# Performance work log

Measured on AMD Instinct MI355X. Metric: run time of the kernel, lower is better.

## Reference

```python
import jax, jax.numpy as jnp
import numpy as np
import math

HEAD_DIM = 64
N_NEWTON_ITER = 6


def _top_k_sum_selection(T, select_number, mask):
    # T: [B,H,N,D]; mask: [B,N] int (True/1 => masked out for selection, per source)
    B, H, N, D = T.shape
    big = jnp.finfo(T.dtype).max
    # select_type == 'sum' -> non-absolute row sums over feature dim, excluding token 0
    somme = jnp.sum(T[:, :, 1:, :], axis=-1)                      # [B,H,N-1]
    somme = jnp.where(mask[:, None, 1:].astype(bool), -big, somme)
    top = jax.lax.top_k(somme, select_number - 1)[1] + 1          # [B,H,M-1]
    top = jnp.concatenate(
        [top, jnp.zeros((B, H, 1), dtype=top.dtype)], axis=-1)    # always keep token 0
    index = jnp.sort(top, axis=-1)                                 # [B,H,M]
    nt = jnp.take_along_axis(T, index[..., None], axis=2)          # [B,H,M,D]
    return nt, index


def _m_matrix_composition(C, r_index):
    # C: [B,H,N,M]; r_index: [B,H,M] -> gather selected rows -> [B,H,M,M]
    return jnp.take_along_axis(C, r_index[..., None], axis=2)


def _iterative_inv(mat, n_iter=N_NEWTON_ITER):
    M = mat.shape[-1]
    I = jnp.eye(M, dtype=mat.dtype)
    Km = mat
    # init_option == 'original': global max of column sums
    V = (1.0 / jnp.max(jnp.sum(Km, axis=-2))) * jnp.swapaxes(Km, -1, -2)
    for _ in range(n_iter):
        KV = jnp.matmul(Km, V)
        V = jnp.matmul(0.25 * V,
                       13.0 * I - jnp.matmul(KV, 15.0 * I - jnp.matmul(KV, 7.0 * I - KV)))
    return V


def setup_inputs() -> dict:
    key = jax.random.key(0)
    k1, k2, k3, k4 = jax.random.split(key, 4)
    B, H, N, D = 4, 8, 4096, 64
    return {
        "Q": jax.random.normal(k1, (B, H, N, D), dtype=jnp.float32),
        "K": jax.random.normal(k2, (B, H, N, D), dtype=jnp.float32),
        "V": jax.random.normal(k3, (B, H, N, D), dtype=jnp.float32),
        "mask": jax.random.randint(k4, (B, N), 0, 2, dtype=jnp.int32),
        "select_number": 64,
    }


def reference(Q, K, V, mask, select_number):
    big = jnp.finfo(Q.dtype).max
    Qs = Q / math.sqrt(HEAD_DIM)
    nc, _ = _top_k_sum_selection(K, select_number, mask)           # [B,H,M,D]
    nr, r_index = _top_k_sum_selection(Qs, select_number, mask)    # [B,H,M,D]
    c = jnp.einsum('bhnd,bhmd->bhnm', Qs, nc)                      # [B,H,N,M]
    r = jnp.einsum('bhmd,bhnd->bhmn', nr, K)                       # [B,H,M,N]
    # forward path fills where ~mask (mask==0 => masked)
    r = jnp.where(mask[:, None, None, :].astype(bool), r, -big)
    kernel_1 = jax.nn.softmax(c, axis=-1)                          # [B,H,N,M]
    u = _m_matrix_composition(kernel_1, r_index)                   # [B,H,M,M]
    kernel_3 = jax.nn.softmax(r, axis=-1)                          # [B,H,M,N]
    kernel_2_inv = _iterative_inv(u)                               # [B,H,M,M]
    X = jnp.matmul(kernel_1, jnp.matmul(kernel_2_inv, jnp.matmul(kernel_3, V)))
    return X
```

## Files before the change

kernel.cpp:

```cpp
#include <hip/hip_runtime.h>
#include <float.h>

#define BB 4
#define HH 8
#define BHN 32
#define NTOK 4096
#define DD 64
#define MM 64
#define PAD 68
#define GPART 16

typedef _Float16 f16;
typedef __attribute__((ext_vector_type(4))) _Float16 f16x4;
typedef __attribute__((ext_vector_type(8))) _Float16 f16x8;
typedef __attribute__((ext_vector_type(4))) float f32x4;

union V8U { f16x8 v; f16x4 q[2]; };

__device__ __forceinline__ void fsplit(float v, f16* h, f16* l) {
  f16 hh = (f16)v;
  *h = hh;
  *l = (f16)(v - (float)hh);
}

__device__ __forceinline__ f32x4 mm2(f16x8 a0, f16x8 a1, f16x8 b0, f16x8 b1) {
  f32x4 c = {0.f, 0.f, 0.f, 0.f};
  c = __builtin_amdgcn_mfma_f32_16x16x32_f16(a0, b0, c, 0, 0, 0);
  c = __builtin_amdgcn_mfma_f32_16x16x32_f16(a1, b1, c, 0, 0, 0);
  return c;
}

template<int LDA, int LDB>
__device__ __forceinline__ void mm_acc(float acc[4][4],
    const float (*A)[LDA], const float (*B)[LDB], int ti, int tj) {
  #pragma unroll
  for (int k4 = 0; k4 < 16; ++k4) {
    float a[4][4], b[4][4];
    #pragma unroll
    for (int x = 0; x < 4; ++x) {
      float4 t = *(const float4*)&A[ti*4+x][k4*4];
      a[x][0]=t.x; a[x][1]=t.y; a[x][2]=t.z; a[x][3]=t.w;
    }
    #pragma unroll
    for (int kk = 0; kk < 4; ++kk) {
      float4 t = *(const float4*)&B[k4*4+kk][tj*4];
      b[kk][0]=t.x; b[kk][1]=t.y; b[kk][2]=t.z; b[kk][3]=t.w;
    }
    #pragma unroll
    for (int kk = 0; kk < 4; ++kk)
      #pragma unroll
      for (int x = 0; x < 4; ++x)
        #pragma unroll
        for (int y = 0; y < 4; ++y)
          acc[x][y] = fmaf(a[x][kk], b[kk][y], acc[x][y]);
  }
}

__global__ __launch_bounds__(256) void k_somme(const float* __restrict__ Kg,
    const float* __restrict__ Qg, const int* __restrict__ mask,
    float* __restrict__ somK, float* __restrict__ somQ) {
  int tid = threadIdx.x;
  int lane = tid & 63;
  long grow = (long)blockIdx.x * 16 + (tid >> 6) * 4 + (lane >> 4);
  int which = grow >= (long)(BHN * NTOK);
  long row = which ? grow - (long)BHN * NTOK : grow;
  int n = (int)(row & (NTOK - 1));
  int bh = (int)(row >> 12);
  int b = bh >> 3;
  const float* src = which ? Qg : Kg;
  float4 v = *((const float4*)(src + row * DD) + (lane & 15));
  float s = v.x + v.y + v.z + v.w;
  s += __shfl_xor(s, 1); s += __shfl_xor(s, 2);
  s += __shfl_xor(s, 4); s += __shfl_xor(s, 8);
  if ((lane & 15) == 0) {
    float out = (n == 0 || mask[b * NTOK + n] != 0) ? -FLT_MAX : s;
    (which ? somQ : somK)[row] = out;
  }
}

__global__ __launch_bounds__(256) void k_select(const float* __restrict__ Kg,
    const float* __restrict__ Qg, const float* __restrict__ somK,
    const float* __restrict__ somQ, float* __restrict__ nc, float* __restrict__ nr,
    unsigned int* __restrict__ sync0) {
  int bh = blockIdx.x;
  int which = blockIdx.y;
  if (which == 0 && bh == 0 && threadIdx.x == 0) {
    #pragma unroll
    for (int i = 0; i < 34; ++i) sync0[i] = 0u;
  }
  __shared__ unsigned int keys[NTOK];
  __shared__ unsigned int wb[4][256];
  __shared__ int wsum[4];
  __shared__ int wsumB[4];
  __shared__ int sh_bin, sh_need;
  __shared__ int sel[MM];
  int tid = threadIdx.x, wave = tid >> 6, lane = tid & 63;
  const float* som = (which ? somQ : somK) + (long)bh * NTOK;
  for (int i = tid; i < NTOK; i += 256) {
    float f = som[i];
    unsigned int u = __float_as_uint(f);
    u = (u & 0x80000000u) ? ~u : (u | 0x80000000u);
    keys[i] = (i == 0) ? 0u : u;
  }
  unsigned int pref = 0; int need = MM - 1;
  for (int pass = 0; pass < 4; ++pass) {
    int shift = 24 - pass * 8;
    unsigned int pm = (pass == 0) ? 0u : (0xFFFFFFFFu << (32 - 8 * pass));
    unsigned int* wbf = (unsigned int*)wb;
    wbf[tid] = 0; wbf[tid + 256] = 0; wbf[tid + 512] = 0; wbf[tid + 768] = 0;
    __syncthreads();
    for (int i = tid; i < NTOK; i += 256) {
      unsigned int k = keys[i];
      if ((k & pm) == pref) atomicAdd(&wb[wave][(k >> shift) & 255], 1u);
    }
    __syncthreads();
    int binr = 255 - tid;
    int cnt = (int)(wb[0][binr] + wb[1][binr] + wb[2][binr] + wb[3][binr]);
    int v = cnt;
    #pragma unroll
    for (int d = 1; d < 64; d <<= 1) {
      int t = __shfl_up(v, d);
      if (lane >= d) v += t;
    }
    if (lane == 63) wsum[wave] = v;
    __syncthreads();
    int off = 0;
    #pragma unroll
    for (int w = 0; w < 4; ++w) off += (w < wave) ? wsum[w] : 0;
    v += off;
    int above = v - cnt;
    if (v >= need && above < need) { sh_bin = binr; sh_need = need - above; }
    __syncthreads();
    pref |= ((unsigned int)sh_bin) << shift;
    need = sh_need;
  }
  unsigned int thr = pref;

  int base = tid * 16;
  int ctie = 0;
  #pragma unroll
  for (int j = 0; j < 16; ++j) ctie += (keys[base + j] == thr);
  int v2 = ctie;
  #pragma unroll
  for (int d = 1; d < 64; d <<= 1) {
    int t = __shfl_up(v2, d);
    if (lane >= d) v2 += t;
  }
  if (lane == 63) wsum[wave] = v2;
  __syncthreads();
  int offt = 0;
  #pragma unroll
  for (int w = 0; w < 4; ++w) offt += (w < wave) ? wsum[w] : 0;
  int tie_excl = v2 + offt - ctie;

  int tieoff = tie_excl, cnt2 = 0;
  #pragma unroll
  for (int j = 0; j < 16; ++j) {
    unsigned int k = keys[base + j];
    int f = (k > thr) ? 1 : 0;
    if (k == thr) { f = (tieoff < need) ? 1 : 0; ++tieoff; }
    if (base + j == 0) f = 1;
    cnt2 += f;
  }
  int v3 = cnt2;
  #pragma unroll
  for (int d = 1; d < 64; d <<= 1) {
    int t = __shfl_up(v3, d);
    if (lane >= d) v3 += t;
  }
  if (lane == 63) wsumB[wave] = v3;
  __syncthreads();
  int offc = 0;
  #pragma unroll
  for (int w = 0; w < 4; ++w) offc += (w < wave) ? wsumB[w] : 0;
  int o = v3 + offc - cnt2;
  tieoff = tie_excl;
  #pragma unroll
  for (int j = 0; j < 16; ++j) {
    unsigned int k = keys[base + j];
    int f = (k > thr) ? 1 : 0;
    if (k == thr) { f = (tieoff < need) ? 1 : 0; ++tieoff; }
    if (base + j == 0) f = 1;
    if (f) sel[o++] = base + j;
  }
  __syncthreads();

  const float* src = which ? Qg : Kg;
  float* dst = (which ? nr : nc) + (long)bh * MM * DD;
  float scale = which ? 0.125f : 1.0f;
  for (int e = tid; e < MM * 16; e += 256) {
    int i = e >> 4, d4 = e & 15;
    float4 v = *(const float4*)&src[((long)bh * NTOK + sel[i]) * DD + d4 * 4];
    v.x *= scale; v.y *= scale; v.z *= scale; v.w *= scale;
    *(float4*)&dst[i * DD + d4 * 4] = v;
  }
}

__device__ void newton_fused(char* smem, const float* __restrict__ nc,
    const float* __restrict__ nr, unsigned int* __restrict__ scal,
    unsigned int* __restrict__ uflag, const float* __restrict__ nump,
    const float* __restrict__ denp, unsigned int* __restrict__ w3cnt,
    float* __restrict__ Zg, int bh) {
  int tid = threadIdx.x;
  float* uL = (float*)(smem + 55296);

  {
    float (*A)[PAD] = (float(*)[PAD])smem;
    float (*BT)[MM] = (float(*)[MM])(smem + 17408);
    float (*cs)[MM] = (float(*)[MM])(smem + 33792);
    if (tid < 256) {
      for (int e = tid; e < 1024; e += 256) {
        int m = e >> 4, d4 = e & 15;
        *(float4*)&A[m][d4*4] = *(const float4*)&nr[(long)bh*MM*DD + m*DD + d4*4];
        float4 c = *(const float4*)&nc[(long)bh*MM*DD + m*DD + d4*4];
        BT[d4*4+0][m] = c.x; BT[d4*4+1][m] = c.y; BT[d4*4+2][m] = c.z; BT[d4*4+3][m] = c.w;
      }
    }
    __syncthreads();
    if (tid < 256) {
      int ti = tid >> 4, tj = tid & 15;
      float acc[4][4] = {};
      mm_acc<PAD, MM>(acc, A, BT, ti, tj);
      float e_[4][4];
      #pragma unroll
      for (int x = 0; x < 4; ++x)
        #pragma unroll
        for (int y = 0; y < 4; ++y) e_[x][y] = expf(acc[x][y]);
      float rsx[4];
      #pragma unroll
      for (int x = 0; x < 4; ++x) {
        rsx[x] = e_[x][0] + e_[x][1] + e_[x][2] + e_[x][3];
        rsx[x] += __shfl_xor(rsx[x], 1); rsx[x] += __shfl_xor(rsx[x], 2);
        rsx[x] += __shfl_xor(rsx[x], 4); rsx[x] += __shfl_xor(rsx[x], 8);
      }
      float cp[4] = {0.f, 0.f, 0.f, 0.f};
      #pragma unroll
      for (int x = 0; x < 4; ++x) {
        float inv = 1.f / rsx[x];
        float v0 = e_[x][0]*inv, v1 = e_[x][1]*inv, v2 = e_[x][2]*inv, v3 = e_[x][3]*inv;
        cp[0] += v0; cp[1] += v1; cp[2] += v2; cp[3] += v3;
        float4 o; o.x = v0; o.y = v1; o.z = v2; o.w = v3;
        *(float4*)&uL[(ti*4+x)*MM + tj*4] = o;
      }
      #pragma unroll
      for (int y = 0; y < 4; ++y) {
        cp[y] += __shfl_xor(cp[y], 16);
        cp[y] += __shfl_xor(cp[y], 32);
      }
      if (((tid >> 4) & 3) == 0) {
        #pragma unroll
        for (int y = 0; y < 4; ++y) cs[tid >> 6][tj*4 + y] = cp[y];
      }
    }
    __syncthreads();
    if (tid < 64) {
      float tot = cs[0][tid] + cs[1][tid] + cs[2][tid] + cs[3][tid];
      for (int off = 32; off; off >>= 1) tot = fmaxf(tot, __shfl_xor(tot, off));
      if (tid == 0) atomicMax(scal, __float_as_uint(tot));
    }
    __syncthreads();
    if (tid == 0)
      __hip_atomic_fetch_add(uflag, 1u, __ATOMIC_RELEASE, __HIP_MEMORY_SCOPE_AGENT);
    if (tid == 0) {
      while (__hip_atomic_load(uflag, __ATOMIC_ACQUIRE, __HIP_MEMORY_SCOPE_AGENT) < 32u)
        __builtin_amdgcn_s_sleep(1);
      unsigned int sv = __hip_atomic_load(scal, __ATOMIC_RELAXED, __HIP_MEMORY_SCOPE_AGENT);
      cs[0][0] = 1.0f / __uint_as_float(sv);
    }
    __syncthreads();
  }
  float c0 = ((float(*)[MM])(smem + 33792))[0][0];
  __syncthreads();

  f16 (*VT_h)[72] = (f16(*)[72])(smem);
  f16 (*Vr_h)[72] = (f16(*)[72])(smem + 9216);
  f16 (*PT_h)[72] = (f16(*)[72])(smem + 18432);
  f16 (*PT_l)[72] = (f16(*)[72])(smem + 27648);
  f16 (*RT_h)[72] = (f16(*)[72])(smem + 36864);
  f16 (*RT_l)[72] = (f16(*)[72])(smem + 46080);
  float (*Vi)[PAD] = (float(*)[PAD])(smem + 36864);
  int wave = tid >> 6, lane = tid & 63;
  int wr = wave >> 1, wc = wave & 1;
  int lm = lane & 15, hi = lane >> 4;

  for (int e = tid; e < 4096; e += 512) {
    int i = e >> 6, j = e & 63;
    f16 h = (f16)(uL[e] * c0);
    VT_h[i][j] = h;
    Vr_h[j][i] = h;
  }
  f16x8 kb_h[2], kb_l[2];
  {
    const float* p = uL + (wr*16 + lm) * 64;
    float kv[16];
    *(float4*)&kv[0]  = *(const float4*)(p + hi*8);
    *(float4*)&kv[4]  = *(const float4*)(p + hi*8 + 4);
    *(float4*)&kv[8]  = *(const float4*)(p + 32 + hi*8);
    *(float4*)&kv[12] = *(const float4*)(p + 36 + hi*8);
    #pragma unroll
    for (int j = 0; j < 8; ++j) {
      f16 h, l;
      fsplit(kv[j], &h, &l);     kb_h[0][j] = h; kb_l[0][j] = l;
      fsplit(kv[8+j], &h, &l);   kb_h[1][j] = h; kb_l[1][j] = l;
    }
  }
  __syncthreads();

  for (int it = 0; it < 6; ++it) {
    const bool last = (it == 5);

    f32x4 st[4];
    #pragma unroll
    for (int g = 0; g < 4; ++g) {
      f16x8 a0 = *(const f16x8*)&VT_h[g*16 + lm][hi*8];
      f16x8 a1 = *(const f16x8*)&VT_h[g*16 + lm][32 + hi*8];
      f32x4 c = mm2(a0, a1, kb_h[0], kb_h[1]);
      if (last) {
        c = __builtin_amdgcn_mfma_f32_16x16x32_f16(a0, kb_l[0], c, 0, 0, 0);
        c = __builtin_amdgcn_mfma_f32_16x16x32_f16(a1, kb_l[1], c, 0, 0, 0);
      }
      st[g] = c;
    }
    f16x8 sa[2];
    #pragma unroll
    for (int g = 0; g < 4; ++g)
      #pragma unroll
      for (int r = 0; r < 4; ++r)
        sa[g >> 1][(g & 1)*4 + r] = (f16)st[g][r];
    #pragma unroll
    for (int g = 0; g < 4; ++g) {
      if ((g >> 1) == wc) {
        #pragma unroll
        for (int r = 0; r < 4; ++r) {
          int i = g*16 + hi*4 + r, j = wr*16 + lm;
          float pv = (i == j ? 7.f : 0.f) - st[g][r];
          if (last) {
            f16 h, l; fsplit(pv, &h, &l);
            PT_h[i][j] = h; PT_l[i][j] = l;
          } else {
            PT_h[i][j] = (f16)pv;
          }
        }
      }
    }
    __syncthreads();

    #pragma unroll
    for (int cc2 = 0; cc2 < 2; ++cc2) {
      int cc = wc*2 + cc2;
      V8U bh0, bh1;
      bh0.q[0] = *(const f16x4*)&PT_h[cc*16 + lm][hi*4];
      bh0.q[1] = *(const f16x4*)&PT_h[cc*16 + lm][16 + hi*4];
      bh1.q[0] = *(const f16x4*)&PT_h[cc*16 + lm][32 + hi*4];
      bh1.q[1] = *(const f16x4*)&PT_h[cc*16 + lm][48 + hi*4];
      f32x4 a = mm2(sa[0], sa[1], bh0.v, bh1.v);
      if (last) {
        V8U bl0, bl1;
        bl0.q[0] = *(const f16x4*)&PT_l[cc*16 + lm][hi*4];
        bl0.q[1] = *(const f16x4*)&PT_l[cc*16 + lm][16 + hi*4];
        bl1.q[0] = *(const f16x4*)&PT_l[cc*16 + lm][32 + hi*4];
        bl1.q[1] = *(const f16x4*)&PT_l[cc*16 + lm][48 + hi*4];
        a = __builtin_amdgcn_mfma_f32_16x16x32_f16(sa[0], bl0.v, a, 0, 0, 0);
        a = __builtin_amdgcn_mfma_f32_16x16x32_f16(sa[1], bl1.v, a, 0, 0, 0);
      }
      f16x4 wh, wl;
      #pragma unroll
      for (int r = 0; r < 4; ++r) {
        int row = wr*16 + hi*4 + r, col = cc*16 + lm;
        float rv = (row == col ? 15.f : 0.f) - a[r];
        if (last) { f16 h, l; fsplit(rv, &h, &l); wh[r] = h; wl[r] = l; }
        else wh[r] = (f16)rv;
      }
      *(f16x4*)&RT_h[cc*16 + lm][wr*16 + hi*4] = wh;
      if (last) *(f16x4*)&RT_l[cc*16 + lm][wr*16 + hi*4] = wl;
    }
    __syncthreads();

    #pragma unroll
    for (int cc2 = 0; cc2 < 2; ++cc2) {
      int cc = wc*2 + cc2;
      V8U bh0, bh1;
      bh0.q[0] = *(const f16x4*)&RT_h[cc*16 + lm][hi*4];
      bh0.q[1] = *(const f16x4*)&RT_h[cc*16 + lm][16 + hi*4];
      bh1.q[0] = *(const f16x4*)&RT_h[cc*16 + lm][32 + hi*4];
      bh1.q[1] = *(const f16x4*)&RT_h[cc*16 + lm][48 + hi*4];
      f32x4 a = mm2(sa[0], sa[1], bh0.v, bh1.v);
      if (last) {
        V8U bl0, bl1;
        bl0.q[0] = *(const f16x4*)&RT_l[cc*16 + lm][hi*4];
        bl0.q[1] = *(const f16x4*)&RT_l[cc*16 + lm][16 + hi*4];
        bl1.q[0] = *(const f16x4*)&RT_l[cc*16 + lm][32 + hi*4];
        bl1.q[1] = *(const f16x4*)&RT_l[cc*16 + lm][48 + hi*4];
        a = __builtin_amdgcn_mfma_f32_16x16x32_f16(sa[0], bl0.v, a, 0, 0, 0);
        a = __builtin_amdgcn_mfma_f32_16x16x32_f16(sa[1], bl1.v, a, 0, 0, 0);
      }
      f16x4 wh, wl;
      #pragma unroll
      for (int r = 0; r < 4; ++r) {
        int row = wr*16 + hi*4 + r, col = cc*16 + lm;
        float wv = (row == col ? 13.f : 0.f) - a[r];
        if (last) { f16 h, l; fsplit(wv, &h, &l); wh[r] = h; wl[r] = l; }
        else wh[r] = (f16)wv;
      }
      *(f16x4*)&PT_h[cc*16 + lm][wr*16 + hi*4] = wh;
      if (last) *(f16x4*)&PT_l[cc*16 + lm][wr*16 + hi*4] = wl;
    }
    __syncthreads();

    f16x8 vh0 = *(const f16x8*)&Vr_h[wr*16 + lm][hi*8];
    f16x8 vh1 = *(const f16x8*)&Vr_h[wr*16 + lm][32 + hi*8];
    #pragma unroll
    for (int cc2 = 0; cc2 < 2; ++cc2) {
      int cc = wc*2 + cc2;
      f16x8 wh0 = *(const f16x8*)&PT_h[cc*16 + lm][hi*8];
      f16x8 wh1 = *(const f16x8*)&PT_h[cc*16 + lm][32 + hi*8];
      f32x4 a = mm2(vh0, vh1, wh0, wh1);
      if (last) {
        f16x8 wl0 = *(const f16x8*)&PT_l[cc*16 + lm][hi*8];
        f16x8 wl1 = *(const f16x8*)&PT_l[cc*16 + lm][32 + hi*8];
        a = __builtin_amdgcn_mfma_f32_16x16x32_f16(vh0, wl0, a, 0, 0, 0);
        a = __builtin_amdgcn_mfma_f32_16x16x32_f16(vh1, wl1, a, 0, 0, 0);
        #pragma unroll
        for (int r = 0; r < 4; ++r)
          Vi[wr*16 + hi*4 + r][cc*16 + lm] = 0.25f * a[r];
      } else {
        f16x4 th;
        #pragma unroll
        for (int r = 0; r < 4; ++r) {
          f16 h = (f16)(0.25f * a[r]);
          Vr_h[wr*16 + hi*4 + r][cc*16 + lm] = h;
          th[r] = h;
        }
        *(f16x4*)&VT_h[cc*16 + lm][wr*16 + hi*4] = th;
      }
    }
    __syncthreads();
  }

  if (tid == 0) {
    while (__hip_atomic_load(&w3cnt[bh], __ATOMIC_ACQUIRE, __HIP_MEMORY_SCOPE_AGENT) < 8u)
      __builtin_amdgcn_s_sleep(1);
  }
  __syncthreads();
  float (*W)[PAD] = (float(*)[PAD])smem;
  float* dn = (float*)(smem + 54272);
  if (tid < 64) {
    float s = 0.f;
    #pragma unroll
    for (int g = 0; g < GPART; ++g) s += denp[((long)bh * GPART + g) * MM + tid];
    dn[tid] = s;
  }
  __syncthreads();
  for (int e = tid; e < 1024; e += 512) {
    int m = e >> 4, d4 = e & 15;
    float4 s = {0.f, 0.f, 0.f, 0.f};
    #pragma unroll
    for (int g = 0; g < GPART; ++g) {
      float4 t = *(const float4*)&nump[((long)bh * GPART + g) * (MM*DD) + m*DD + d4*4];
      s.x += t.x; s.y += t.y; s.z += t.z; s.w += t.w;
    }
    float inv = 1.f / dn[m];
    s.x *= inv; s.y *= inv; s.z *= inv; s.w *= inv;
    *(float4*)&W[m][d4*4] = s;
  }
  __syncthreads();
  if (tid < 256) {
    int ti = tid >> 4, tj = tid & 15;
    float acc[4][4] = {};
    mm_acc<PAD, PAD>(acc, Vi, W, ti, tj);
    #pragma unroll
    for (int x = 0; x < 4; ++x) {
      float4 o; o.x = acc[x][0]; o.y = acc[x][1]; o.z = acc[x][2]; o.w = acc[x][3];
      *(float4*)&Zg[(long)bh*MM*DD + (ti*4+x)*DD + tj*4] = o;
    }
  }
}

__device__ void w3_dev(char* smem, const float* __restrict__ Kg,
    const float* __restrict__ Vg, const int* __restrict__ maskg,
    const float* __restrict__ nr, float* __restrict__ nump,
    float* __restrict__ denp, unsigned int* __restrict__ w3cnt, int idx) {
  int bh = idx >> 3, grp = idx & 7, b = bh >> 3;
  int tid = threadIdx.x;
  int half = tid >> 8, t = tid & 255;
  f16 (*Ks)[72] = (f16(*)[72])(smem + half * 18432);
  f16 (*Vs)[72] = (f16(*)[72])(smem + half * 18432 + 9216);
  float* kmul = (float*)(smem + 36864) + half * 64;
  int lane = tid & 63;
  int lm = lane & 15, hi = lane >> 4;
  int wv = t >> 6;
  int m0 = wv * 16;
  int gslot = grp * 2 + half;

  f16x8 nrf[2];
  {
    const float* p = nr + (long)bh*MM*DD + (long)(m0 + lm)*DD + hi*8;
    float4 q0 = *(const float4*)p;
    float4 q1 = *(const float4*)(p + 4);
    float4 q2 = *(const float4*)(p + 32);
    float4 q3 = *(const float4*)(p + 36);
    nrf[0][0]=(f16)q0.x; nrf[0][1]=(f16)q0.y; nrf[0][2]=(f16)q0.z; nrf[0][3]=(f16)q0.w;
    nrf[0][4]=(f16)q1.x; nrf[0][5]=(f16)q1.y; nrf[0][6]=(f16)q1.z; nrf[0][7]=(f16)q1.w;
    nrf[1][0]=(f16)q2.x; nrf[1][1]=(f16)q2.y; nrf[1][2]=(f16)q2.z; nrf[1][3]=(f16)q2.w;
    nrf[1][4]=(f16)q3.x; nrf[1][5]=(f16)q3.y; nrf[1][6]=(f16)q3.z; nrf[1][7]=(f16)q3.w;
  }

  f32x4 nacc[4];
  #pragma unroll
  for (int dt = 0; dt < 4; ++dt) nacc[dt] = (f32x4){0.f, 0.f, 0.f, 0.f};
  float dsum = 0.f;

  for (int sc = 0; sc < 4; ++sc) {
    int n0c = (gslot * 4 + sc) * 64;
    if (sc) __syncthreads();
    for (int s = t; s < 1024; s += 256) {
      int row = s >> 4, c4 = s & 15;
      float4 kv = *(const float4*)&Kg[((long)bh*NTOK + n0c + row)*DD + c4*4];
      float4 vv = *(const float4*)&Vg[((long)bh*NTOK + n0c + row)*DD + c4*4];
      f16x4 kk = {(f16)kv.x, (f16)kv.y, (f16)kv.z, (f16)kv.w};
      f16x4 vv4 = {(f16)vv.x, (f16)vv.y, (f16)vv.z, (f16)vv.w};
      *(f16x4*)&Ks[row][c4*4] = kk;
      *(f16x4*)&Vs[row][c4*4] = vv4;
    }
    if (t < 64) kmul[t] = maskg[b * NTOK + n0c + t] ? 1.f : 0.f;
    __syncthreads();

    f32x4 stv[4];
    #pragma unroll
    for (int g = 0; g < 4; ++g) {
      f16x8 a0 = *(const f16x8*)&Ks[g*16 + lm][hi*8];
      f16x8 a1 = *(const f16x8*)&Ks[g*16 + lm][32 + hi*8];
      stv[g] = mm2(a0, a1, nrf[0], nrf[1]);
    }
    f16x8 pa[2];
    #pragma unroll
    for (int g = 0; g < 4; ++g) {
      #pragma unroll
      for (int r = 0; r < 4; ++r) {
        float p = __expf(stv[g][r]) * kmul[g*16 + hi*4 + r];
        dsum += p;
        pa[g >> 1][(g & 1)*4 + r] = (f16)p;
      }
    }
    #pragma unroll
    for (int dt = 0; dt < 4; ++dt) {
      f16x8 vb0, vb1;
      #pragma unroll
      for (int j = 0; j < 8; ++j) {
        int nrow = hi*4 + (j & 3) + 16*(j >> 2);
        vb0[j] = Vs[nrow][dt*16 + lm];
        vb1[j] = Vs[32 + nrow][dt*16 + lm];
      }
      nacc[dt] = __builtin_amdgcn_mfma_f32_16x16x32_f16(pa[0], vb0, nacc[dt], 0, 0, 0);
      nacc[dt] = __builtin_amdgcn_mfma_f32_16x16x32_f16(pa[1], vb1, nacc[dt], 0, 0, 0);
    }
  }
  float* pnum = nump + ((long)bh * GPART + gslot) * (MM * DD);
  #pragma unroll
  for (int dt = 0; dt < 4; ++dt)
    #pragma unroll
    for (int r = 0; r < 4; ++r)
      pnum[(m0 + hi*4 + r)*DD + dt*16 + lm] = nacc[dt][r];
  float d2 = dsum + __shfl_xor(dsum, 16);
  d2 += __shfl_xor(d2, 32);
  if (lane < 16)
    denp[((long)bh * GPART + gslot) * MM + m0 + lane] = d2;
  __syncthreads();
  if (tid == 0)
    __hip_atomic_fetch_add(&w3cnt[bh], 1u, __ATOMIC_RELEASE, __HIP_MEMORY_SCOPE_AGENT);
}

__global__ __launch_bounds__(512, 4) void k_fuse(
    const float* __restrict__ nc, const float* __restrict__ nr,
    unsigned int* __restrict__ scal, unsigned int* __restrict__ uflag,
    const float* __restrict__ Kg, const float* __restrict__ Vg,
    const int* __restrict__ maskg,
    float* __restrict__ nump, float* __restrict__ denp,
    unsigned int* __restrict__ w3cnt, float* __restrict__ Zg) {
  __shared__ __align__(16) char smem[71680];
  if (blockIdx.x < 32)
    newton_fused(smem, nc, nr, scal, uflag, nump, denp, w3cnt, Zg, blockIdx.x);
  else
    w3_dev(smem, Kg, Vg, maskg, nr, nump, denp, w3cnt, blockIdx.x - 32);
}

__global__ __launch_bounds__(256) void k_final(const float* __restrict__ Qg,
    const float* __restrict__ nc, const float* __restrict__ Zg, float* __restrict__ Xg) {
  int bh = blockIdx.x, chunk = blockIdx.y;
  int tid = threadIdx.x;
  int wave = tid >> 6, lane = tid & 63;
  int lm = lane & 15, hi = lane >> 4;
  int n0 = chunk * 64;
  __shared__ f16 Qs[64][72];
  __shared__ f16 Ncs[64][72];
  __shared__ f16 Zs[64][72];
  for (int s = tid; s < 1024; s += 256) {
    int row = s >> 4, c4 = s & 15;
    float4 q = *(const float4*)&Qg[((long)bh*NTOK + n0 + row)*DD + c4*4];
    f16x4 qq = {(f16)(q.x*0.125f), (f16)(q.y*0.125f), (f16)(q.z*0.125f), (f16)(q.w*0.125f)};
    *(f16x4*)&Qs[row][c4*4] = qq;
    float4 cv = *(const float4*)&nc[(long)bh*MM*DD + row*DD + c4*4];
    f16x4 cc = {(f16)cv.x, (f16)cv.y, (f16)cv.z, (f16)cv.w};
    *(f16x4*)&Ncs[row][c4*4] = cc;
    float4 zv = *(const float4*)&Zg[(long)bh*MM*DD + row*DD + c4*4];
    f16x4 zz = {(f16)zv.x, (f16)zv.y, (f16)zv.z, (f16)zv.w};
    *(f16x4*)&Zs[row][c4*4] = zz;
  }
  __syncthreads();

  f16x8 qb0 = *(const f16x8*)&Qs[wave*16 + lm][hi*8];
  f16x8 qb1 = *(const f16x8*)&Qs[wave*16 + lm][32 + hi*8];
  f32x4 stv[4];
  #pragma unroll
  for (int mt = 0; mt < 4; ++mt) {
    f16x8 a0 = *(const f16x8*)&Ncs[mt*16 + lm][hi*8];
    f16x8 a1 = *(const f16x8*)&Ncs[mt*16 + lm][32 + hi*8];
    stv[mt] = mm2(a0, a1, qb0, qb1);
  }
  f16x8 pa[2];
  float dsum = 0.f;
  #pragma unroll
  for (int mt = 0; mt < 4; ++mt) {
    #pragma unroll
    for (int r = 0; r < 4; ++r) {
      float p = __expf(stv[mt][r]);
      dsum += p;
      pa[mt >> 1][(mt & 1)*4 + r] = (f16)p;
    }
  }
  float dtot = dsum + __shfl_xor(dsum, 16);
  dtot += __shfl_xor(dtot, 32);
  f32x4 xacc[4];
  #pragma unroll
  for (int dt = 0; dt < 4; ++dt) {
    f16x8 zb0, zb1;
    #pragma unroll
    for (int j = 0; j < 8; ++j) {
      int mrow = hi*4 + (j & 3) + 16*(j >> 2);
      zb0[j] = Zs[mrow][dt*16 + lm];
      zb1[j] = Zs[32 + mrow][dt*16 + lm];
    }
    f32x4 c = {0.f, 0.f, 0.f, 0.f};
    c = __builtin_amdgcn_mfma_f32_16x16x32_f16(pa[0], zb0, c, 0, 0, 0);
    c = __builtin_amdgcn_mfma_f32_16x16x32_f16(pa[1], zb1, c, 0, 0, 0);
    xacc[dt] = c;
  }
  float rn[4];
  #pragma unroll
  for (int r = 0; r < 4; ++r) rn[r] = 1.f / __shfl(dtot, hi*4 + r);
  #pragma unroll
  for (int dt = 0; dt < 4; ++dt)
    #pragma unroll
    for (int r = 0; r < 4; ++r)
      Xg[((long)bh*NTOK + n0 + wave*16 + hi*4 + r)*DD + dt*16 + lm] = xacc[dt][r] * rn[r];
}

extern "C" void kernel_launch(void* const* d_in, const int* in_sizes, int n_in,
                              void* d_out, int out_size, void* d_ws, size_t ws_size,
                              hipStream_t stream) {
  (void)in_sizes; (void)n_in; (void)out_size; (void)ws_size;
  const float* Qp = (const float*)d_in[0];
  const float* Kp = (const float*)d_in[1];
  const float* Vp = (const float*)d_in[2];
  const int* maskp = (const int*)d_in[3];
  float* out = (float*)d_out;

  float* wsf = (float*)d_ws;
  float* NUMP = wsf;
  float* DENP = NUMP + (long)BHN * GPART * MM * DD;
  unsigned int* SYNC = (unsigned int*)(DENP + BHN * GPART * MM);
  float* NC = (float*)(SYNC + 64);
  float* NR = NC + BHN * MM * DD;
  float* Zb = NR + BHN * MM * DD;
  float* SK = Zb + BHN * MM * DD;
  float* SQ = SK + BHN * NTOK;

  unsigned int* SCAL = SYNC;
  unsigned int* UFLAG = SYNC + 1;
  unsigned int* W3CNT = SYNC + 2;

  k_somme<<<16384, 256, 0, stream>>>(Kp, Qp, maskp, SK, SQ);
  k_select<<<dim3(32, 2), 256, 0, stream>>>(Kp, Qp, SK, SQ, NC, NR, SYNC);
  k_fuse<<<32 + 256, 512, 0, stream>>>(NC, NR, SCAL, UFLAG, Kp, Vp, maskp,
                                       NUMP, DENP, W3CNT, Zb);
  k_final<<<dim3(32, 64), 256, 0, stream>>>(Qp, NC, Zb, out);
}
```

Before: 80.14 us.

## Move U-matrix softmax into select kernel, drop in-kernel grid barrier

k_select now uses one 512-thread block per head that selects both K and Q top-k together. It then builds the 64x64 softmax matrix u and the global column-sum max directly from shared memory and writes u to global memory. The Newton blocks in k_fuse read u and the scale instead of recomputing them, which removes the spin-wait barrier across 32 blocks and lowers the shared memory needed per block. Zeroing the sync counters moves into k_somme. In exchange, k_select becomes a heavier serial stage made of only 32 blocks.

```diff
diff --git a/kernel.cpp b/kernel.cpp
--- a/kernel.cpp
+++ b/kernel.cpp
@@ -58,8 +58,13 @@
 
 __global__ __launch_bounds__(256) void k_somme(const float* __restrict__ Kg,
     const float* __restrict__ Qg, const int* __restrict__ mask,
-    float* __restrict__ somK, float* __restrict__ somQ) {
+    float* __restrict__ somK, float* __restrict__ somQ,
+    unsigned int* __restrict__ syncp) {
   int tid = threadIdx.x;
+  if (blockIdx.x == 0 && tid == 0) {
+    #pragma unroll
+    for (int i = 0; i < 34; ++i) syncp[i] = 0u;
+  }
   int lane = tid & 63;
   long grow = (long)blockIdx.x * 16 + (tid >> 6) * 4 + (lane >> 4);
   int which = grow >= (long)(BHN * NTOK);
@@ -78,25 +83,22 @@
   }
 }
 
-__global__ __launch_bounds__(256) void k_select(const float* __restrict__ Kg,
+__global__ __launch_bounds__(512) void k_select(const float* __restrict__ Kg,
     const float* __restrict__ Qg, const float* __restrict__ somK,
     const float* __restrict__ somQ, float* __restrict__ nc, float* __restrict__ nr,
-    unsigned int* __restrict__ sync0) {
+    float* __restrict__ ug, unsigned int* __restrict__ scal) {
+  __shared__ __align__(16) char sm[40960];
+  __shared__ int wsum[2][4], wsumB[2][4], sh_bin[2], sh_need[2];
+  __shared__ int sel[2][MM];
   int bh = blockIdx.x;
-  int which = blockIdx.y;
-  if (which == 0 && bh == 0 && threadIdx.x == 0) {
-    #pragma unroll
-    for (int i = 0; i < 34; ++i) sync0[i] = 0u;
-  }
-  __shared__ unsigned int keys[NTOK];
-  __shared__ unsigned int wb[4][256];
-  __shared__ int wsum[4];
-  __shared__ int wsumB[4];
-  __shared__ int sh_bin, sh_need;
-  __shared__ int sel[MM];
-  int tid = threadIdx.x, wave = tid >> 6, lane = tid & 63;
-  const float* som = (which ? somQ : somK) + (long)bh * NTOK;
-  for (int i = tid; i < NTOK; i += 256) {
+  int tid = threadIdx.x;
+  int half = tid >> 8, t = tid & 255;
+  int lane = tid & 63, wv = (tid >> 6) & 3;
+  unsigned int* keys = (unsigned int*)sm + half * 4096;
+  unsigned int* wbp  = (unsigned int*)(sm + 32768) + half * 1024;
+
+  const float* som = (half ? somQ : somK) + (long)bh * NTOK;
+  for (int i = t; i < NTOK; i += 256) {
     float f = som[i];
     unsigned int u = __float_as_uint(f);
     u = (u & 0x80000000u) ? ~u : (u | 0x80000000u);
@@ -106,51 +108,50 @@
   for (int pass = 0; pass < 4; ++pass) {
     int shift = 24 - pass * 8;
     unsigned int pm = (pass == 0) ? 0u : (0xFFFFFFFFu << (32 - 8 * pass));
-    unsigned int* wbf = (unsigned int*)wb;
-    wbf[tid] = 0; wbf[tid + 256] = 0; wbf[tid + 512] = 0; wbf[tid + 768] = 0;
-    __syncthreads();
-    for (int i = tid; i < NTOK; i += 256) {
+    wbp[t] = 0; wbp[t + 256] = 0; wbp[t + 512] = 0; wbp[t + 768] = 0;
+    __syncthreads();
+    for (int i = t; i < NTOK; i += 256) {
       unsigned int k = keys[i];
-      if ((k & pm) == pref) atomicAdd(&wb[wave][(k >> shift) & 255], 1u);
-    }
-    __syncthreads();
-    int binr = 255 - tid;
-    int cnt = (int)(wb[0][binr] + wb[1][binr] + wb[2][binr] + wb[3][binr]);
+      if ((k & pm) == pref) atomicAdd(&wbp[wv * 256 + ((k >> shift) & 255)], 1u);
+    }
+    __syncthreads();
+    int binr = 255 - t;
+    int cnt = (int)(wbp[binr] + wbp[256 + binr] + wbp[512 + binr] + wbp[768 + binr]);
     int v = cnt;
     #pragma unroll
     for (int d = 1; d < 64; d <<= 1) {
-      int t = __shfl_up(v, d);
-      if (lane >= d) v += t;
-    }
-    if (lane == 63) wsum[wave] = v;
+      int tt = __shfl_up(v, d);
+      if (lane >= d) v += tt;
+    }
+    if (lane == 63) wsum[half][wv] = v;
     __syncthreads();
     int off = 0;
     #pragma unroll
-    for (int w = 0; w < 4; ++w) off += (w < wave) ? wsum[w] : 0;
+    for (int w = 0; w < 4; ++w) off += (w < wv) ? wsum[half][w] : 0;
     v += off;
     int above = v - cnt;
-    if (v >= need && above < need) { sh_bin = binr; sh_need = need - above; }
-    __syncthreads();
-    pref |= ((unsigned int)sh_bin) << shift;
-    need = sh_need;
+    if (v >= need && above < need) { sh_bin[half] = binr; sh_need[half] = need - above; }
+    __syncthreads();
+    pref |= ((unsigned int)sh_bin[half]) << shift;
+    need = sh_need[half];
   }
   unsigned int thr = pref;
 
-  int base = tid * 16;
+  int base = t * 16;
   int ctie = 0;
   #pragma unroll
   for (int j = 0; j < 16; ++j) ctie += (keys[base + j] == thr);
   int v2 = ctie;
   #pragma unroll
   for (int d = 1; d < 64; d <<= 1) {
-    int t = __shfl_up(v2, d);
-    if (lane >= d) v2 += t;
-  }
-  if (lane == 63) wsum[wave] = v2;
+    int tt = __shfl_up(v2, d);
+    if (lane >= d) v2 += tt;
+  }
+  if (lane == 63) wsum[half][wv] = v2;
   __syncthreads();
   int offt = 0;
   #pragma unroll
-  for (int w = 0; w < 4; ++w) offt += (w < wave) ? wsum[w] : 0;
+  for (int w = 0; w < 4; ++w) offt += (w < wv) ? wsum[half][w] : 0;
   int tie_excl = v2 + offt - ctie;
 
   int tieoff = tie_excl, cnt2 = 0;
@@ -165,14 +166,14 @@
   int v3 = cnt2;
   #pragma unroll
   for (int d = 1; d < 64; d <<= 1) {
-    int t = __shfl_up(v3, d);
-    if (lane >= d) v3 += t;
-  }
-  if (lane == 63) wsumB[wave] = v3;
+    int tt = __shfl_up(v3, d);
+    if (lane >= d) v3 += tt;
+  }
+  if (lane == 63) wsumB[half][wv] = v3;
   __syncthreads();
   int offc = 0;
   #pragma unroll
-  for (int w = 0; w < 4; ++w) offc += (w < wave) ? wsumB[w] : 0;
+  for (int w = 0; w < 4; ++w) offc += (w < wv) ? wsumB[half][w] : 0;
   int o = v3 + offc - cnt2;
   tieoff = tie_excl;
   #pragma unroll
@@ -181,97 +182,77 @@
     int f = (k > thr) ? 1 : 0;
     if (k == thr) { f = (tieoff < need) ? 1 : 0; ++tieoff; }
     if (base + j == 0) f = 1;
-    if (f) sel[o++] = base + j;
-  }
-  __syncthreads();
-
-  const float* src = which ? Qg : Kg;
-  float* dst = (which ? nr : nc) + (long)bh * MM * DD;
-  float scale = which ? 0.125f : 1.0f;
-  for (int e = tid; e < MM * 16; e += 256) {
+    if (f) sel[half][o++] = base + j;
+  }
+  __syncthreads();
+
+  float (*A)[PAD] = (float(*)[PAD])sm;
+  float (*BT)[MM] = (float(*)[MM])(sm + 17408);
+  float (*cs)[MM] = (float(*)[MM])(sm + 33792);
+  const float* src = half ? Qg : Kg;
+  float* dst = (half ? nr : nc) + (long)bh * MM * DD;
+  float scale = half ? 0.125f : 1.0f;
+  for (int e = t; e < 1024; e += 256) {
     int i = e >> 4, d4 = e & 15;
-    float4 v = *(const float4*)&src[((long)bh * NTOK + sel[i]) * DD + d4 * 4];
+    float4 v = *(const float4*)&src[((long)bh * NTOK + sel[half][i]) * DD + d4 * 4];
     v.x *= scale; v.y *= scale; v.z *= scale; v.w *= scale;
     *(float4*)&dst[i * DD + d4 * 4] = v;
-  }
-}
-
-__device__ void newton_fused(char* smem, const float* __restrict__ nc,
-    const float* __restrict__ nr, unsigned int* __restrict__ scal,
-    unsigned int* __restrict__ uflag, const float* __restrict__ nump,
+    if (half) {
+      *(float4*)&A[i][d4*4] = v;
+    } else {
+      BT[d4*4+0][i] = v.x; BT[d4*4+1][i] = v.y;
+      BT[d4*4+2][i] = v.z; BT[d4*4+3][i] = v.w;
+    }
+  }
+  __syncthreads();
+
+  if (tid < 256) {
+    int ti = tid >> 4, tj = tid & 15;
+    float acc[4][4] = {};
+    mm_acc<PAD, MM>(acc, A, BT, ti, tj);
+    float e_[4][4];
+    #pragma unroll
+    for (int x = 0; x < 4; ++x)
+      #pragma unroll
+      for (int y = 0; y < 4; ++y) e_[x][y] = expf(acc[x][y]);
+    float rsx[4];
+    #pragma unroll
+    for (int x = 0; x < 4; ++x) {
+      rsx[x] = e_[x][0] + e_[x][1] + e_[x][2] + e_[x][3];
+      rsx[x] += __shfl_xor(rsx[x], 1); rsx[x] += __shfl_xor(rsx[x], 2);
+      rsx[x] += __shfl_xor(rsx[x], 4); rsx[x] += __shfl_xor(rsx[x], 8);
+    }
+    float cp[4] = {0.f, 0.f, 0.f, 0.f};
+    #pragma unroll
+    for (int x = 0; x < 4; ++x) {
+      float inv = 1.f / rsx[x];
+      float v0 = e_[x][0]*inv, v1 = e_[x][1]*inv, v2 = e_[x][2]*inv, v3 = e_[x][3]*inv;
+      cp[0] += v0; cp[1] += v1; cp[2] += v2; cp[3] += v3;
+      float4 ov; ov.x = v0; ov.y = v1; ov.z = v2; ov.w = v3;
+      *(float4*)&ug[(long)bh*MM*MM + (ti*4+x)*MM + tj*4] = ov;
+    }
+    #pragma unroll
+    for (int y = 0; y < 4; ++y) {
+      cp[y] += __shfl_xor(cp[y], 16);
+      cp[y] += __shfl_xor(cp[y], 32);
+    }
+    if (((tid >> 4) & 3) == 0) {
+      #pragma unroll
+      for (int y = 0; y < 4; ++y) cs[tid >> 6][tj*4 + y] = cp[y];
+    }
+  }
+  __syncthreads();
+  if (tid < 64) {
+    float tot = cs[0][tid] + cs[1][tid] + cs[2][tid] + cs[3][tid];
+    for (int off = 32; off; off >>= 1) tot = fmaxf(tot, __shfl_xor(tot, off));
+    if (tid == 0) atomicMax(scal, __float_as_uint(tot));
+  }
+}
+
+__device__ void newton_fused(char* smem, const float* __restrict__ ug,
+    const unsigned int* __restrict__ scal, const float* __restrict__ nump,
     const float* __restrict__ denp, unsigned int* __restrict__ w3cnt,
     float* __restrict__ Zg, int bh) {
-  int tid = threadIdx.x;
-  float* uL = (float*)(smem + 55296);
-
-  {
-    float (*A)[PAD] = (float(*)[PAD])smem;
-    float (*BT)[MM] = (float(*)[MM])(smem + 17408);
-    float (*cs)[MM] = (float(*)[MM])(smem + 33792);
-    if (tid < 256) {
-      for (int e = tid; e < 1024; e += 256) {
-        int m = e >> 4, d4 = e & 15;
-        *(float4*)&A[m][d4*4] = *(const float4*)&nr[(long)bh*MM*DD + m*DD + d4*4];
-        float4 c = *(const float4*)&nc[(long)bh*MM*DD + m*DD + d4*4];
-        BT[d4*4+0][m] = c.x; BT[d4*4+1][m] = c.y; BT[d4*4+2][m] = c.z; BT[d4*4+3][m] = c.w;
-      }
-    }
-    __syncthreads();
-    if (tid < 256) {
-      int ti = tid >> 4, tj = tid & 15;
-      float acc[4][4] = {};
-      mm_acc<PAD, MM>(acc, A, BT, ti, tj);
-      float e_[4][4];
-      #pragma unroll
-      for (int x = 0; x < 4; ++x)
-        #pragma unroll
-        for (int y = 0; y < 4; ++y) e_[x][y] = expf(acc[x][y]);
-      float rsx[4];
-      #pragma unroll
-      for (int x = 0; x < 4; ++x) {
-        rsx[x] = e_[x][0] + e_[x][1] + e_[x][2] + e_[x][3];
-        rsx[x] += __shfl_xor(rsx[x], 1); rsx[x] += __shfl_xor(rsx[x], 2);
-        rsx[x] += __shfl_xor(rsx[x], 4); rsx[x] += __shfl_xor(rsx[x], 8);
-      }
-      float cp[4] = {0.f, 0.f, 0.f, 0.f};
-      #pragma unroll
-      for (int x = 0; x < 4; ++x) {
-        float inv = 1.f / rsx[x];
-        float v0 = e_[x][0]*inv, v1 = e_[x][1]*inv, v2 = e_[x][2]*inv, v3 = e_[x][3]*inv;
-        cp[0] += v0; cp[1] += v1; cp[2] += v2; cp[3] += v3;
-        float4 o; o.x = v0; o.y = v1; o.z = v2; o.w = v3;
-        *(float4*)&uL[(ti*4+x)*MM + tj*4] = o;
-      }
-      #pragma unroll
-      for (int y = 0; y < 4; ++y) {
-        cp[y] += __shfl_xor(cp[y], 16);
-        cp[y] += __shfl_xor(cp[y], 32);
-      }
-      if (((tid >> 4) & 3) == 0) {
-        #pragma unroll
-        for (int y = 0; y < 4; ++y) cs[tid >> 6][tj*4 + y] = cp[y];
-      }
-    }
-    __syncthreads();
-    if (tid < 64) {
-      float tot = cs[0][tid] + cs[1][tid] + cs[2][tid] + cs[3][tid];
-      for (int off = 32; off; off >>= 1) tot = fmaxf(tot, __shfl_xor(tot, off));
-      if (tid == 0) atomicMax(scal, __float_as_uint(tot));
-    }
-    __syncthreads();
-    if (tid == 0)
-      __hip_atomic_fetch_add(uflag, 1u, __ATOMIC_RELEASE, __HIP_MEMORY_SCOPE_AGENT);
-    if (tid == 0) {
-      while (__hip_atomic_load(uflag, __ATOMIC_ACQUIRE, __HIP_MEMORY_SCOPE_AGENT) < 32u)
-        __builtin_amdgcn_s_sleep(1);
-      unsigned int sv = __hip_atomic_load(scal, __ATOMIC_RELAXED, __HIP_MEMORY_SCOPE_AGENT);
-      cs[0][0] = 1.0f / __uint_as_float(sv);
-    }
-    __syncthreads();
-  }
-  float c0 = ((float(*)[MM])(smem + 33792))[0][0];
-  __syncthreads();
-
   f16 (*VT_h)[72] = (f16(*)[72])(smem);
   f16 (*Vr_h)[72] = (f16(*)[72])(smem + 9216);
   f16 (*PT_h)[72] = (f16(*)[72])(smem + 18432);
@@ -279,19 +260,22 @@
   f16 (*RT_h)[72] = (f16(*)[72])(smem + 36864);
   f16 (*RT_l)[72] = (f16(*)[72])(smem + 46080);
   float (*Vi)[PAD] = (float(*)[PAD])(smem + 36864);
+  int tid = threadIdx.x;
   int wave = tid >> 6, lane = tid & 63;
   int wr = wave >> 1, wc = wave & 1;
   int lm = lane & 15, hi = lane >> 4;
 
+  float c0 = 1.0f / __uint_as_float(scal[0]);
+  const float* pu = ug + (long)bh * MM * MM;
   for (int e = tid; e < 4096; e += 512) {
     int i = e >> 6, j = e & 63;
-    f16 h = (f16)(uL[e] * c0);
+    f16 h = (f16)(pu[e] * c0);
     VT_h[i][j] = h;
     Vr_h[j][i] = h;
   }
   f16x8 kb_h[2], kb_l[2];
   {
-    const float* p = uL + (wr*16 + lm) * 64;
+    const float* p = pu + (wr*16 + lm) * 64;
     float kv[16];
     *(float4*)&kv[0]  = *(const float4*)(p + hi*8);
     *(float4*)&kv[4]  = *(const float4*)(p + hi*8 + 4);
@@ -571,15 +555,14 @@
 }
 
 __global__ __launch_bounds__(512, 4) void k_fuse(
-    const float* __restrict__ nc, const float* __restrict__ nr,
-    unsigned int* __restrict__ scal, unsigned int* __restrict__ uflag,
+    const float* __restrict__ ug, const unsigned int* __restrict__ scal,
     const float* __restrict__ Kg, const float* __restrict__ Vg,
-    const int* __restrict__ maskg,
+    const int* __restrict__ maskg, const float* __restrict__ nr,
     float* __restrict__ nump, float* __restrict__ denp,
     unsigned int* __restrict__ w3cnt, float* __restrict__ Zg) {
-  __shared__ __align__(16) char smem[71680];
+  __shared__ __align__(16) char smem[55296];
   if (blockIdx.x < 32)
-    newton_fused(smem, nc, nr, scal, uflag, nump, denp, w3cnt, Zg, blockIdx.x);
+    newton_fused(smem, ug, scal, nump, denp, w3cnt, Zg, blockIdx.x);
   else
     w3_dev(smem, Kg, Vg, maskg, nr, nump, denp, w3cnt, blockIdx.x - 32);
 }
@@ -669,19 +652,19 @@
   float* NUMP = wsf;
   float* DENP = NUMP + (long)BHN * GPART * MM * DD;
   unsigned int* SYNC = (unsigned int*)(DENP + BHN * GPART * MM);
-  float* NC = (float*)(SYNC + 64);
+  float* UG = (float*)(SYNC + 64);
+  float* NC = UG + BHN * MM * MM;
   float* NR = NC + BHN * MM * DD;
   float* Zb = NR + BHN * MM * DD;
   float* SK = Zb + BHN * MM * DD;
   float* SQ = SK + BHN * NTOK;
 
   unsigned int* SCAL = SYNC;
-  unsigned int* UFLAG = SYNC + 1;
-  unsigned int* W3CNT = SYNC + 2;
-
-  k_somme<<<16384, 256, 0, stream>>>(Kp, Qp, maskp, SK, SQ);
-  k_select<<<dim3(32, 2), 256, 0, stream>>>(Kp, Qp, SK, SQ, NC, NR, SYNC);
-  k_fuse<<<32 + 256, 512, 0, stream>>>(NC, NR, SCAL, UFLAG, Kp, Vp, maskp,
+  unsigned int* W3CNT = SYNC + 1;
+
+  k_somme<<<16384, 256, 0, stream>>>(Kp, Qp, maskp, SK, SQ, SYNC);
+  k_select<<<32, 512, 0, stream>>>(Kp, Qp, SK, SQ, NC, NR, UG, SCAL);
+  k_fuse<<<32 + 256, 512, 0, stream>>>(UG, SCAL, Kp, Vp, maskp, NR,
                                        NUMP, DENP, W3CNT, Zb);
   k_final<<<dim3(32, 64), 256, 0, stream>>>(Qp, NC, Zb, out);
 }
```

New measurement: 92.99 us. 16.0% more time.
